# Kernel tuning notes

Hardware: AMD Instinct MI355X
Metric: run time of the kernel (lower is better)

The kernel has to match this reference:

```python
import jax, jax.numpy as jnp
import numpy as np

B, S, E, H = 4, 2048, 2048, 16
D = E // H  # 128


def _rope(x, sin, cos):
    # x: (B, S, H, D); sin/cos: (S, D//2)
    x1, x2 = jnp.split(x, 2, axis=-1)
    c = cos[None, :, None, :]
    s = sin[None, :, None, :]
    return jnp.concatenate([x1 * c - x2 * s, x1 * s + x2 * c], axis=-1)


def setup_inputs() -> dict:
    key = jax.random.key(0)
    ks = jax.random.split(key, 12)
    inp = {
        "x_q": jax.random.normal(ks[0], (B, S, E), jnp.float32),
        "x_kv": jax.random.normal(ks[1], (B, S, E), jnp.float32),
        "Wq": jax.random.normal(ks[2], (E, E), jnp.float32) / np.sqrt(E),
        "bq": jnp.zeros((E,), jnp.float32),
        "Wk": jax.random.normal(ks[3], (E, E), jnp.float32) / np.sqrt(E),
        "bk": jnp.zeros((E,), jnp.float32),
        "Wv": jax.random.normal(ks[4], (E, E), jnp.float32) / np.sqrt(E),
        "bv": jnp.zeros((E,), jnp.float32),
        "Wo": jax.random.normal(ks[5], (E, E), jnp.float32) / np.sqrt(E),
        "bo": jnp.zeros((E,), jnp.float32),
        "angles": jax.random.uniform(ks[6], (2, S, D // 2), jnp.float32),
        "attn_mask": jnp.ones((B, S), jnp.int32),
        "causal": 0,
        "k_rope": 1,
    }
    return inp


def reference(x_q, x_kv, Wq, bq, Wk, bk, Wv, bv, Wo, bo, angles, attn_mask, causal, k_rope):
    sin, cos = angles[0], angles[1]
    q = (x_q @ Wq.T + bq).reshape(B, S, H, D)
    k = (x_kv @ Wk.T + bk).reshape(B, S, H, D)
    v = (x_kv @ Wv.T + bv).reshape(B, S, H, D)
    q = _rope(q, sin, cos)
    if k_rope:
        k = _rope(k, sin, cos)
    # scaled dot-product attention, heads leading: (B, H, S, S)
    scores = jnp.einsum("bqhd,bkhd->bhqk", q, k) / np.sqrt(D).astype(np.float32)
    mask = attn_mask.astype(bool)[:, None, None, :]  # (B,1,1,S_kv)
    if causal:
        cm = jnp.tril(jnp.ones((S, S), bool))[None, None]
        mask = mask & cm
    scores = jnp.where(mask, scores, jnp.finfo(scores.dtype).min)
    probs = jax.nn.softmax(scores, axis=-1)
    attn = jnp.einsum("bhqk,bkhd->bqhd", probs, v).reshape(B, S, E)
    return attn @ Wo.T + bo
```

## Files before the change

### kernel.cpp

```cpp
#include <hip/hip_runtime.h>
#include <hip/hip_bf16.h>


typedef __bf16 bf16;
typedef __bf16 bf16x8 __attribute__((ext_vector_type(8)));
typedef __bf16 bf16x4 __attribute__((ext_vector_type(4)));
typedef __bf16 bf16x2 __attribute__((ext_vector_type(2)));
typedef float  f32x4  __attribute__((ext_vector_type(4)));
typedef float  f32x16 __attribute__((ext_vector_type(16)));

constexpr int Bc = 4, Sc = 2048, Ec = 2048, Hc = 16, Dc = 128;
constexpr int Mc = Bc * Sc;

__device__ __forceinline__ void async16(const void* g, void* l) {
  __builtin_amdgcn_global_load_lds(
      (const __attribute__((address_space(1))) void*)g,
      (__attribute__((address_space(3))) void*)l, 16, 0, 0);
}

__device__ __forceinline__ unsigned int pkbf(float a, float b) {
  union { bf16x2 v; unsigned int u; } c;
  c.v[0] = (bf16)a; c.v[1] = (bf16)b;
  return c.u;
}

__device__ __forceinline__ int swzb32(int r, int kb) {
  int b = r * 64 + kb;
  return b ^ (((b >> 9) & 1) << 5);
}

__global__ void cvt_multi(const float* s0, const float* s1, const float* s2, const float* s3,
                          bf16* d0, bf16* d1, bf16* d2, bf16* d3, int n8) {
  const float* src; bf16* dst;
  switch (blockIdx.y) {
    case 0:  src = s0; dst = d0; break;
    case 1:  src = s1; dst = d1; break;
    case 2:  src = s2; dst = d2; break;
    default: src = s3; dst = d3; break;
  }
  int i = blockIdx.x * blockDim.x + threadIdx.x;
  const int stride = gridDim.x * blockDim.x;
  for (; i < n8; i += stride) {
    const float4 a = *((const float4*)src + (size_t)i * 2);
    const float4 b = *((const float4*)src + (size_t)i * 2 + 1);
    bf16x8 o;
    o[0] = (bf16)a.x; o[1] = (bf16)a.y; o[2] = (bf16)a.z; o[3] = (bf16)a.w;
    o[4] = (bf16)b.x; o[5] = (bf16)b.y; o[6] = (bf16)b.z; o[7] = (bf16)b.w;
    *(bf16x8*)(dst + (size_t)i * 8) = o;
  }
}

template <int OUT_BF16>
__global__ __launch_bounds__(512, 2) void gemm8(
    const bf16* __restrict__ A, const bf16* __restrict__ Bm,
    const float* __restrict__ bias, void* __restrict__ Cout, int Mblocks)
{
  __shared__ __align__(16) bf16 lds[3 * 16384];
  const int tid = threadIdx.x;
  const int w = tid >> 6, lane = tid & 63;
  const int l15 = lane & 15, l16 = lane >> 4;
  const int wm = w >> 2, wn = w & 3;
  const int id = blockIdx.x;
  const int nwg = Mblocks * 8, cpx = nwg >> 3;
  const int swz = (id & 7) * cpx + (id >> 3);
  const int by = swz >> 3, bx = swz & 7;
  const long m0 = (long)by * 256, n0 = (long)bx * 256;
  constexpr int NT = 64;

  auto stA = [&](int buf, long kt, int j) {
    int c = w * 128 + j * 64 + lane;
    int cs = c ^ (((c >> 5) & 1) << 1);
    async16(A + (m0 + (cs >> 2)) * 2048 + kt + (cs & 3) * 8,
            &lds[buf * 16384 + c * 8]);
  };
  auto stB = [&](int buf, long kt, int j) {
    int c = w * 128 + j * 64 + lane;
    int cs = c ^ (((c >> 5) & 1) << 1);
    async16(Bm + (n0 + (cs >> 2)) * 2048 + kt + (cs & 3) * 8,
            &lds[buf * 16384 + 8192 + c * 8]);
  };

  f32x4 acc[8][4];
#pragma unroll
  for (int a = 0; a < 8; ++a)
#pragma unroll
    for (int b = 0; b < 4; ++b) acc[a][b] = f32x4{0.f, 0.f, 0.f, 0.f};

  stA(0, 0, 0); stA(0, 0, 1); stB(0, 0, 0); stB(0, 0, 1);
  stA(1, 32, 0); stA(1, 32, 1); stB(1, 32, 0); stB(1, 32, 1);
  asm volatile("s_waitcnt vmcnt(4)" ::: "memory");
  __builtin_amdgcn_s_barrier();

  int cur = 0, nx = 2;
  for (int t = 0; t < NT; ++t) {
    const char* Ab = (const char*)&lds[cur * 16384];
    const char* Bb = Ab + 16384;
    const long ktn = (long)(t + 2) * 32;
    const bool pf = (t < NT - 2);

    bf16x8 af[8], bf0[2];
#pragma unroll
    for (int mf = 0; mf < 8; ++mf)
      af[mf] = *(const bf16x8*)(Ab + swzb32(wm * 128 + mf * 16 + l15, l16 * 16));
#pragma unroll
    for (int nf = 0; nf < 2; ++nf)
      bf0[nf] = *(const bf16x8*)(Bb + swzb32(wn * 64 + nf * 16 + l15, l16 * 16));
    if (pf) { stA(nx, ktn, 0); stA(nx, ktn, 1); }
    asm volatile("" ::: "memory");
    __builtin_amdgcn_s_barrier();
    __builtin_amdgcn_s_setprio(1);
#pragma unroll
    for (int mf = 0; mf < 8; ++mf)
#pragma unroll
      for (int nf = 0; nf < 2; ++nf)
        acc[mf][nf] = __builtin_amdgcn_mfma_f32_16x16x32_bf16(af[mf], bf0[nf], acc[mf][nf], 0, 0, 0);
    __builtin_amdgcn_s_setprio(0);
    __builtin_amdgcn_s_barrier();

    bf16x8 bf1[2];
#pragma unroll
    for (int nf = 0; nf < 2; ++nf)
      bf1[nf] = *(const bf16x8*)(Bb + swzb32(wn * 64 + (2 + nf) * 16 + l15, l16 * 16));
    if (pf) { stB(nx, ktn, 0); stB(nx, ktn, 1); }
    asm volatile("" ::: "memory");
    __builtin_amdgcn_s_barrier();
    __builtin_amdgcn_s_setprio(1);
#pragma unroll
    for (int mf = 0; mf < 8; ++mf)
#pragma unroll
      for (int nf = 0; nf < 2; ++nf)
        acc[mf][2 + nf] = __builtin_amdgcn_mfma_f32_16x16x32_bf16(af[mf], bf1[nf], acc[mf][2 + nf], 0, 0, 0);
    __builtin_amdgcn_s_setprio(0);
    if (t < NT - 2)       { asm volatile("s_waitcnt vmcnt(4)" ::: "memory"); }
    else if (t == NT - 2) { asm volatile("s_waitcnt vmcnt(0)" ::: "memory"); }
    __builtin_amdgcn_s_barrier();
    cur = (cur == 2) ? 0 : cur + 1;
    nx  = (nx  == 2) ? 0 : nx  + 1;
  }

#pragma unroll
  for (int mf = 0; mf < 8; ++mf)
#pragma unroll
    for (int nf = 0; nf < 4; ++nf) {
      const long m = m0 + wm * 128 + mf * 16 + l16 * 4;
      const long n = n0 + wn * 64 + nf * 16 + l15;
      const float bv = bias[n];
#pragma unroll
      for (int i = 0; i < 4; ++i) {
        float v = acc[mf][nf][i] + bv;
        if (OUT_BF16) ((bf16*)Cout)[(m + i) * 2048 + n] = (bf16)v;
        else          ((float*)Cout)[(m + i) * 2048 + n] = v;
      }
    }
}

__global__ void rope_kernel(bf16* __restrict__ x, const float* __restrict__ angles,
                            const int* __restrict__ flag, int force)
{
  if (!force && flag[0] == 0) return;
  const int t = threadIdx.x;
  const long R = (long)blockIdx.x * 64 + (t >> 2);
  const int d0 = (t & 3) * 16;
  const long s = (R / Hc) % Sc;
  bf16* rowp = x + R * Dc;
  bf16x8 lo0 = *(bf16x8*)(rowp + d0);
  bf16x8 lo1 = *(bf16x8*)(rowp + d0 + 8);
  bf16x8 hi0 = *(bf16x8*)(rowp + d0 + 64);
  bf16x8 hi1 = *(bf16x8*)(rowp + d0 + 72);
  const float* sp = angles + s * 64 + d0;
  const float* cp = angles + 131072 + s * 64 + d0;
  bf16x8 a0, a1, b0, b1;
#pragma unroll
  for (int j = 0; j < 8; ++j) {
    float c = cp[j], sn = sp[j];
    float x1 = (float)lo0[j], x2 = (float)hi0[j];
    a0[j] = (bf16)(x1 * c - x2 * sn);
    b0[j] = (bf16)(x1 * sn + x2 * c);
    float c1 = cp[j + 8], sn1 = sp[j + 8];
    float y1 = (float)lo1[j], y2 = (float)hi1[j];
    a1[j] = (bf16)(y1 * c1 - y2 * sn1);
    b1[j] = (bf16)(y1 * sn1 + y2 * c1);
  }
  *(bf16x8*)(rowp + d0)      = a0;
  *(bf16x8*)(rowp + d0 + 8)  = a1;
  *(bf16x8*)(rowp + d0 + 64) = b0;
  *(bf16x8*)(rowp + d0 + 72) = b1;
}

__global__ void transpose_v(const bf16* __restrict__ v0, bf16* __restrict__ Vt)
{
  __shared__ __align__(16) bf16 T[64 * 128];
  const int t = threadIdx.x;
  const int bh = blockIdx.y, b = bh >> 4, h = bh & 15;
  const int s0 = blockIdx.x * 64;
#pragma unroll
  for (int it = 0; it < 4; ++it) {
    int slot = it * 256 + t;
    int r = slot >> 4, g = slot & 15;
    async16(v0 + ((size_t)(b * Sc + s0 + r) * Hc + h) * Dc + ((g ^ (r & 15)) << 3),
            &T[slot * 8]);
  }
  __syncthreads();
  const int d = t >> 1, half = t & 1;
  bf16x8 pk[4];
#pragma unroll
  for (int j = 0; j < 32; ++j) {
    int sl = half * 32 + j;
    pk[j >> 3][j & 7] = T[sl * 128 + (((d >> 3) ^ (sl & 15)) << 3) + (d & 7)];
  }
  bf16* op = Vt + ((size_t)bh * Dc + d) * Sc + s0 + half * 32;
#pragma unroll
  for (int v = 0; v < 4; ++v) *(bf16x8*)(op + v * 8) = pk[v];
}

__global__ __launch_bounds__(256, 2) void attn_kernel(
    const bf16* __restrict__ q0, const bf16* __restrict__ k0,
    const bf16* __restrict__ vt, const int* __restrict__ mask,
    const int* __restrict__ causal_p, const float* __restrict__ angles,
    bf16* __restrict__ attn_out)
{
  __shared__ __align__(16) bf16 Ks[2][64 * 128];
  __shared__ __align__(16) bf16 Vs[2][128 * 64];

  const int tid = threadIdx.x, wid = tid >> 6, lane = tid & 63;
  const int l31 = lane & 31, h = lane >> 5;
  const int id = blockIdx.x;
  const int swz = (id & 7) * 128 + (id >> 3);
  const int bh = swz >> 4, qb = swz & 15;
  const int b = bh >> 4, hh = bh & 15;
  const int q_glob = qb * 128 + wid * 32 + l31;
  const int causal_f = causal_p[0];
  const float SC = 0.08838834764831845f * 1.4426950408889634f;
  const float NEG = -3.0e38f;

  auto stageKV = [&](int kv0s, int bufs) {
#pragma unroll
    for (int it = 0; it < 4; ++it) {
      int g = it * 256 + tid;
      int r = g >> 4, gp = g & 15;
      async16(k0 + ((size_t)(b * Sc + kv0s + r) * Hc + hh) * Dc + ((gp ^ (r & 15)) << 3),
              &Ks[bufs][g * 8]);
    }
#pragma unroll
    for (int it = 0; it < 4; ++it) {
      int g = it * 256 + tid;
      int r = g >> 3, gp = g & 7;
      async16(vt + ((size_t)bh * Dc + r) * Sc + kv0s + ((gp ^ (r & 7)) << 3),
              &Vs[bufs][g * 8]);
    }
  };

  bf16x8 qf[8];
  {
    const bf16* qrow = q0 + ((size_t)(b * Sc + q_glob) * Hc + hh) * Dc;
#pragma unroll
    for (int dc = 0; dc < 4; ++dc) {
      bf16x8 lo = *(const bf16x8*)(qrow + dc * 16 + h * 8);
      bf16x8 hi = *(const bf16x8*)(qrow + (dc + 4) * 16 + h * 8);
      const float* sp = angles + (size_t)q_glob * 64 + dc * 16 + h * 8;
      union { float4 v[2]; float f[8]; } sn, cs;
      sn.v[0] = ((const float4*)sp)[0];
      sn.v[1] = ((const float4*)sp)[1];
      cs.v[0] = ((const float4*)(sp + 131072))[0];
      cs.v[1] = ((const float4*)(sp + 131072))[1];
#pragma unroll
      for (int j = 0; j < 8; ++j) {
        float x1 = (float)lo[j], x2 = (float)hi[j];
        qf[dc][j]     = (bf16)(SC * (x1 * cs.f[j] - x2 * sn.f[j]));
        qf[dc + 4][j] = (bf16)(SC * (x1 * sn.f[j] + x2 * cs.f[j]));
      }
    }
  }

  f32x16 o[4];
#pragma unroll
  for (int db = 0; db < 4; ++db)
#pragma unroll
    for (int r = 0; r < 16; ++r) o[db][r] = 0.f;
  float mrun = NEG, lrun = 0.f;

  stageKV(0, 0);
  const int mv0 = mask[b * Sc + lane];
  asm volatile("s_waitcnt vmcnt(0)" ::: "memory");
  __builtin_amdgcn_s_barrier();
  unsigned long long mbits = __ballot(mv0 != 0);
  int cur = 0;

  for (int kv0 = 0; kv0 < Sc; kv0 += 64) {
    const int kvn = kv0 + 64;
    unsigned long long mbits_next = ~0ull;
    if (kvn < Sc) {
      const int mvn = mask[b * Sc + kvn + lane];
      mbits_next = __ballot(mvn != 0);
      stageKV(kvn, cur ^ 1);
    }

#pragma unroll
    for (int kvb = 0; kvb < 2; ++kvb) {
      f32x16 s;
#pragma unroll
      for (int r = 0; r < 16; ++r) s[r] = 0.f;
      __builtin_amdgcn_s_setprio(1);
#pragma unroll
      for (int dc = 0; dc < 8; ++dc) {
        bf16x8 kf = *(const bf16x8*)&Ks[cur][(kvb * 32 + l31) * 128 +
                                           (((dc * 2 + h) ^ (l31 & 15)) << 3)];
        s = __builtin_amdgcn_mfma_f32_32x32x16_bf16(kf, qf[dc], s, 0, 0, 0);
      }
      __builtin_amdgcn_s_setprio(0);
      if (mbits != ~0ull) {
#pragma unroll
        for (int r = 0; r < 16; ++r) {
          int off = kvb * 32 + (r & 3) + 8 * (r >> 2) + 4 * h;
          if (!((mbits >> off) & 1)) s[r] = NEG;
        }
      }
      if (causal_f) {
#pragma unroll
        for (int r = 0; r < 16; ++r) {
          int kvg = kv0 + kvb * 32 + (r & 3) + 8 * (r >> 2) + 4 * h;
          if (kvg > q_glob) s[r] = NEG;
        }
      }
      float tmax = s[0];
#pragma unroll
      for (int r = 1; r < 16; ++r) tmax = fmaxf(tmax, s[r]);
      tmax = fmaxf(tmax, __shfl_xor(tmax, 32));
      if (!__all(tmax <= mrun + 8.0f)) {
        const float mnew = fmaxf(mrun, tmax);
        const float alpha = __builtin_amdgcn_exp2f(mrun - mnew);
#pragma unroll
        for (int db = 0; db < 4; ++db)
#pragma unroll
          for (int r = 0; r < 16; ++r) o[db][r] *= alpha;
        lrun *= alpha;
        mrun = mnew;
      }
      float rs = 0.f;
#pragma unroll
      for (int r = 0; r < 16; ++r) {
        s[r] = __builtin_amdgcn_exp2f(s[r] - mrun);
        rs += s[r];
      }
      rs += __shfl_xor(rs, 32);
      lrun += rs;
      unsigned int dw0 = pkbf(s[0], s[1]),   dw1 = pkbf(s[2], s[3]);
      unsigned int dw2 = pkbf(s[4], s[5]),   dw3 = pkbf(s[6], s[7]);
      unsigned int dw4 = pkbf(s[8], s[9]),   dw5 = pkbf(s[10], s[11]);
      unsigned int dw6 = pkbf(s[12], s[13]), dw7 = pkbf(s[14], s[15]);
      asm volatile("v_permlane32_swap_b32 %0, %1" : "+v"(dw0), "+v"(dw2));
      asm volatile("v_permlane32_swap_b32 %0, %1" : "+v"(dw1), "+v"(dw3));
      asm volatile("v_permlane32_swap_b32 %0, %1" : "+v"(dw4), "+v"(dw6));
      asm volatile("v_permlane32_swap_b32 %0, %1" : "+v"(dw5), "+v"(dw7));
      union { unsigned int u[4]; bf16x8 v; } pf0, pf1;
      pf0.u[0] = dw0; pf0.u[1] = dw1; pf0.u[2] = dw2; pf0.u[3] = dw3;
      pf1.u[0] = dw4; pf1.u[1] = dw5; pf1.u[2] = dw6; pf1.u[3] = dw7;
      __builtin_amdgcn_s_setprio(1);
#pragma unroll
      for (int ksb = 0; ksb < 2; ++ksb) {
        const bf16x8 pfv = ksb ? pf1.v : pf0.v;
#pragma unroll
        for (int db = 0; db < 4; ++db) {
          const int dr = db * 32 + l31;
          bf16x8 vb = *(const bf16x8*)&Vs[cur][dr * 64 +
                          ((((kvb * 2 + ksb) * 2 + h) ^ (dr & 7)) << 3)];
          o[db] = __builtin_amdgcn_mfma_f32_32x32x16_bf16(vb, pfv, o[db], 0, 0, 0);
        }
      }
      __builtin_amdgcn_s_setprio(0);
    }

    asm volatile("s_waitcnt vmcnt(0)" ::: "memory");
    __builtin_amdgcn_s_barrier();
    cur ^= 1;
    mbits = mbits_next;
  }

  const float inv = 1.0f / lrun;
  bf16* orow = attn_out + ((size_t)(b * Sc + q_glob) * Hc + hh) * Dc;
#pragma unroll
  for (int db = 0; db < 4; ++db)
#pragma unroll
    for (int rq = 0; rq < 4; ++rq) {
      bf16x4 st;
#pragma unroll
      for (int i = 0; i < 4; ++i) st[i] = (bf16)(o[db][rq * 4 + i] * inv);
      *(bf16x4*)(orow + db * 32 + rq * 8 + 4 * h) = st;
    }
}

extern "C" void kernel_launch(void* const* d_in, const int* in_sizes, int n_in,
                              void* d_out, int out_size, void* d_ws, size_t ws_size,
                              hipStream_t stream)
{
  const float* x_q    = (const float*)d_in[0];
  const float* x_kv   = (const float*)d_in[1];
  const float* Wq     = (const float*)d_in[2];
  const float* bq     = (const float*)d_in[3];
  const float* Wk     = (const float*)d_in[4];
  const float* bk     = (const float*)d_in[5];
  const float* Wv     = (const float*)d_in[6];
  const float* bv     = (const float*)d_in[7];
  const float* Wo     = (const float*)d_in[8];
  const float* bo     = (const float*)d_in[9];
  const float* angles = (const float*)d_in[10];
  const int*   amask  = (const int*)d_in[11];
  const int*   causal = (const int*)d_in[12];
  const int*   k_rope = (const int*)d_in[13];
  float* out = (float*)d_out;

  char* ws = (char*)d_ws;
  const size_t MB32 = (size_t)33554432;
  bf16* xq16  = (bf16*)(ws);
  bf16* xkv16 = (bf16*)(ws + MB32);
  bf16* wq16  = (bf16*)(ws + 2 * MB32);
  bf16* wk16  = wq16 + 4194304;
  bf16* wv16  = wk16 + 4194304;
  bf16* wo16  = wv16 + 4194304;
  bf16* q0    = (bf16*)(ws + 3 * MB32);
  bf16* k0    = (bf16*)(ws + 4 * MB32);
  bf16* v0    = (bf16*)(ws + 5 * MB32);
  bf16* Vt     = xq16;
  bf16* attn16 = xkv16;

  cvt_multi<<<dim3(1024, 2), 256, 0, stream>>>(x_q, x_kv, x_q, x_kv,
                                               xq16, xkv16, xq16, xkv16, Mc * Ec / 8);
  cvt_multi<<<dim3(256, 4), 256, 0, stream>>>(Wq, Wk, Wv, Wo,
                                              wq16, wk16, wv16, wo16, Ec * Ec / 8);

  const int gemmBlocks = (Mc / 256) * (Ec / 256);
  gemm8<1><<<gemmBlocks, 512, 0, stream>>>(xq16,  wq16, bq, q0, Mc / 256);
  gemm8<1><<<gemmBlocks, 512, 0, stream>>>(xkv16, wk16, bk, k0, Mc / 256);
  gemm8<1><<<gemmBlocks, 512, 0, stream>>>(xkv16, wv16, bv, v0, Mc / 256);

  rope_kernel<<<2048, 256, 0, stream>>>(k0, angles, k_rope, 0);
  transpose_v<<<dim3(Sc / 64, Bc * Hc), 256, 0, stream>>>(v0, Vt);

  attn_kernel<<<1024, 256, 0, stream>>>(q0, k0, Vt, amask, causal, angles, attn16);

  gemm8<0><<<gemmBlocks, 512, 0, stream>>>(attn16, wo16, bo, out, Mc / 256);
}
```

Measured before the change: 531.9 us.

## Fuse V transpose into GEMM epilogue, deepen GEMM pipeline, restage attention V

The V projection GEMM now writes its output directly in head-major transposed layout, which removes the separate transpose kernel and the intermediate V buffer round trip. The GEMM prefetch ring grows from three to four LDS stages to hide more load latency. The attention kernel now single-buffers V, staging it per tile and waiting on it only after the first QK/softmax chunk, which cuts LDS use so the kernel can target three blocks per CU. In exchange, the transposed epilogue issues strided 8-byte stores, and the 128KB GEMM LDS footprint may no longer allow two blocks per CU.

Measured after the change: 864.7 us. +62.6%, slower.

```diff
diff --git a/kernel.cpp b/kernel.cpp
--- a/kernel.cpp
+++ b/kernel.cpp
@@ -50,12 +50,12 @@
   }
 }
 
-template <int OUT_BF16>
+template <int OUT>
 __global__ __launch_bounds__(512, 2) void gemm8(
     const bf16* __restrict__ A, const bf16* __restrict__ Bm,
     const float* __restrict__ bias, void* __restrict__ Cout, int Mblocks)
 {
-  __shared__ __align__(16) bf16 lds[3 * 16384];
+  __shared__ __align__(16) bf16 lds[4 * 16384];
   const int tid = threadIdx.x;
   const int w = tid >> 6, lane = tid & 63;
   const int l15 = lane & 15, l16 = lane >> 4;
@@ -86,17 +86,18 @@
 #pragma unroll
     for (int b = 0; b < 4; ++b) acc[a][b] = f32x4{0.f, 0.f, 0.f, 0.f};
 
-  stA(0, 0, 0); stA(0, 0, 1); stB(0, 0, 0); stB(0, 0, 1);
+  stA(0, 0, 0);  stA(0, 0, 1);  stB(0, 0, 0);  stB(0, 0, 1);
   stA(1, 32, 0); stA(1, 32, 1); stB(1, 32, 0); stB(1, 32, 1);
-  asm volatile("s_waitcnt vmcnt(4)" ::: "memory");
+  stA(2, 64, 0); stA(2, 64, 1); stB(2, 64, 0); stB(2, 64, 1);
+  asm volatile("s_waitcnt vmcnt(8)" ::: "memory");
   __builtin_amdgcn_s_barrier();
 
-  int cur = 0, nx = 2;
+  int cur = 0, nx = 3;
   for (int t = 0; t < NT; ++t) {
     const char* Ab = (const char*)&lds[cur * 16384];
     const char* Bb = Ab + 16384;
-    const long ktn = (long)(t + 2) * 32;
-    const bool pf = (t < NT - 2);
+    const long ktn = (long)(t + 3) * 32;
+    const bool pf = (t < NT - 3);
 
     bf16x8 af[8], bf0[2];
 #pragma unroll
@@ -131,11 +132,12 @@
       for (int nf = 0; nf < 2; ++nf)
         acc[mf][2 + nf] = __builtin_amdgcn_mfma_f32_16x16x32_bf16(af[mf], bf1[nf], acc[mf][2 + nf], 0, 0, 0);
     __builtin_amdgcn_s_setprio(0);
-    if (t < NT - 2)       { asm volatile("s_waitcnt vmcnt(4)" ::: "memory"); }
+    if (t < NT - 3)       { asm volatile("s_waitcnt vmcnt(8)" ::: "memory"); }
+    else if (t == NT - 3) { asm volatile("s_waitcnt vmcnt(4)" ::: "memory"); }
     else if (t == NT - 2) { asm volatile("s_waitcnt vmcnt(0)" ::: "memory"); }
     __builtin_amdgcn_s_barrier();
-    cur = (cur == 2) ? 0 : cur + 1;
-    nx  = (nx  == 2) ? 0 : nx  + 1;
+    cur = (cur + 1) & 3;
+    nx  = (nx + 1) & 3;
   }
 
 #pragma unroll
@@ -145,11 +147,20 @@
       const long m = m0 + wm * 128 + mf * 16 + l16 * 4;
       const long n = n0 + wn * 64 + nf * 16 + l15;
       const float bv = bias[n];
-#pragma unroll
-      for (int i = 0; i < 4; ++i) {
-        float v = acc[mf][nf][i] + bv;
-        if (OUT_BF16) ((bf16*)Cout)[(m + i) * 2048 + n] = (bf16)v;
-        else          ((float*)Cout)[(m + i) * 2048 + n] = v;
+      if (OUT == 2) {
+        const long bb = m >> 11, ss = m & 2047;
+        const long head = n >> 7, d = n & 127;
+        bf16x4 st;
+#pragma unroll
+        for (int i = 0; i < 4; ++i) st[i] = (bf16)(acc[mf][nf][i] + bv);
+        *(bf16x4*)((bf16*)Cout + ((((bb << 4) + head) << 7) + d) * 2048 + ss) = st;
+      } else {
+#pragma unroll
+        for (int i = 0; i < 4; ++i) {
+          float v = acc[mf][nf][i] + bv;
+          if (OUT == 1) ((bf16*)Cout)[(m + i) * 2048 + n] = (bf16)v;
+          else          ((float*)Cout)[(m + i) * 2048 + n] = v;
+        }
       }
     }
 }
@@ -187,40 +198,14 @@
   *(bf16x8*)(rowp + d0 + 72) = b1;
 }
 
-__global__ void transpose_v(const bf16* __restrict__ v0, bf16* __restrict__ Vt)
-{
-  __shared__ __align__(16) bf16 T[64 * 128];
-  const int t = threadIdx.x;
-  const int bh = blockIdx.y, b = bh >> 4, h = bh & 15;
-  const int s0 = blockIdx.x * 64;
-#pragma unroll
-  for (int it = 0; it < 4; ++it) {
-    int slot = it * 256 + t;
-    int r = slot >> 4, g = slot & 15;
-    async16(v0 + ((size_t)(b * Sc + s0 + r) * Hc + h) * Dc + ((g ^ (r & 15)) << 3),
-            &T[slot * 8]);
-  }
-  __syncthreads();
-  const int d = t >> 1, half = t & 1;
-  bf16x8 pk[4];
-#pragma unroll
-  for (int j = 0; j < 32; ++j) {
-    int sl = half * 32 + j;
-    pk[j >> 3][j & 7] = T[sl * 128 + (((d >> 3) ^ (sl & 15)) << 3) + (d & 7)];
-  }
-  bf16* op = Vt + ((size_t)bh * Dc + d) * Sc + s0 + half * 32;
-#pragma unroll
-  for (int v = 0; v < 4; ++v) *(bf16x8*)(op + v * 8) = pk[v];
-}
-
-__global__ __launch_bounds__(256, 2) void attn_kernel(
+__global__ __launch_bounds__(256, 3) void attn_kernel(
     const bf16* __restrict__ q0, const bf16* __restrict__ k0,
     const bf16* __restrict__ vt, const int* __restrict__ mask,
     const int* __restrict__ causal_p, const float* __restrict__ angles,
     bf16* __restrict__ attn_out)
 {
   __shared__ __align__(16) bf16 Ks[2][64 * 128];
-  __shared__ __align__(16) bf16 Vs[2][128 * 64];
+  __shared__ __align__(16) bf16 Vs[128 * 64];
 
   const int tid = threadIdx.x, wid = tid >> 6, lane = tid & 63;
   const int l31 = lane & 31, h = lane >> 5;
@@ -233,7 +218,7 @@
   const float SC = 0.08838834764831845f * 1.4426950408889634f;
   const float NEG = -3.0e38f;
 
-  auto stageKV = [&](int kv0s, int bufs) {
+  auto stageK = [&](int kv0s, int bufs) {
 #pragma unroll
     for (int it = 0; it < 4; ++it) {
       int g = it * 256 + tid;
@@ -241,12 +226,14 @@
       async16(k0 + ((size_t)(b * Sc + kv0s + r) * Hc + hh) * Dc + ((gp ^ (r & 15)) << 3),
               &Ks[bufs][g * 8]);
     }
+  };
+  auto stageV = [&](int kv0s) {
 #pragma unroll
     for (int it = 0; it < 4; ++it) {
       int g = it * 256 + tid;
       int r = g >> 3, gp = g & 7;
       async16(vt + ((size_t)bh * Dc + r) * Sc + kv0s + ((gp ^ (r & 7)) << 3),
-              &Vs[bufs][g * 8]);
+              &Vs[g * 8]);
     }
   };
 
@@ -279,96 +266,108 @@
     for (int r = 0; r < 16; ++r) o[db][r] = 0.f;
   float mrun = NEG, lrun = 0.f;
 
-  stageKV(0, 0);
+  stageK(0, 0);
   const int mv0 = mask[b * Sc + lane];
   asm volatile("s_waitcnt vmcnt(0)" ::: "memory");
   __builtin_amdgcn_s_barrier();
   unsigned long long mbits = __ballot(mv0 != 0);
   int cur = 0;
 
+  union pfu { unsigned int u[4]; bf16x8 v; };
+  auto qk_sm_pack = [&](int kv0_, int kvb, unsigned long long mb, pfu& pf0, pfu& pf1) {
+    f32x16 s;
+#pragma unroll
+    for (int r = 0; r < 16; ++r) s[r] = 0.f;
+    __builtin_amdgcn_s_setprio(1);
+#pragma unroll
+    for (int dc = 0; dc < 8; ++dc) {
+      bf16x8 kf = *(const bf16x8*)&Ks[cur][(kvb * 32 + l31) * 128 +
+                                         (((dc * 2 + h) ^ (l31 & 15)) << 3)];
+      s = __builtin_amdgcn_mfma_f32_32x32x16_bf16(kf, qf[dc], s, 0, 0, 0);
+    }
+    __builtin_amdgcn_s_setprio(0);
+    if (mb != ~0ull) {
+#pragma unroll
+      for (int r = 0; r < 16; ++r) {
+        int off = kvb * 32 + (r & 3) + 8 * (r >> 2) + 4 * h;
+        if (!((mb >> off) & 1)) s[r] = NEG;
+      }
+    }
+    if (causal_f) {
+#pragma unroll
+      for (int r = 0; r < 16; ++r) {
+        int kvg = kv0_ + kvb * 32 + (r & 3) + 8 * (r >> 2) + 4 * h;
+        if (kvg > q_glob) s[r] = NEG;
+      }
+    }
+    float tmax = s[0];
+#pragma unroll
+    for (int r = 1; r < 16; ++r) tmax = fmaxf(tmax, s[r]);
+    tmax = fmaxf(tmax, __shfl_xor(tmax, 32));
+    if (!__all(tmax <= mrun + 8.0f)) {
+      const float mnew = fmaxf(mrun, tmax);
+      const float alpha = __builtin_amdgcn_exp2f(mrun - mnew);
+#pragma unroll
+      for (int db = 0; db < 4; ++db)
+#pragma unroll
+        for (int r = 0; r < 16; ++r) o[db][r] *= alpha;
+      lrun *= alpha;
+      mrun = mnew;
+    }
+    float rs = 0.f;
+#pragma unroll
+    for (int r = 0; r < 16; ++r) {
+      s[r] = __builtin_amdgcn_exp2f(s[r] - mrun);
+      rs += s[r];
+    }
+    rs += __shfl_xor(rs, 32);
+    lrun += rs;
+    unsigned int dw0 = pkbf(s[0], s[1]),   dw1 = pkbf(s[2], s[3]);
+    unsigned int dw2 = pkbf(s[4], s[5]),   dw3 = pkbf(s[6], s[7]);
+    unsigned int dw4 = pkbf(s[8], s[9]),   dw5 = pkbf(s[10], s[11]);
+    unsigned int dw6 = pkbf(s[12], s[13]), dw7 = pkbf(s[14], s[15]);
+    asm volatile("v_permlane32_swap_b32 %0, %1" : "+v"(dw0), "+v"(dw2));
+    asm volatile("v_permlane32_swap_b32 %0, %1" : "+v"(dw1), "+v"(dw3));
+    asm volatile("v_permlane32_swap_b32 %0, %1" : "+v"(dw4), "+v"(dw6));
+    asm volatile("v_permlane32_swap_b32 %0, %1" : "+v"(dw5), "+v"(dw7));
+    pf0.u[0] = dw0; pf0.u[1] = dw1; pf0.u[2] = dw2; pf0.u[3] = dw3;
+    pf1.u[0] = dw4; pf1.u[1] = dw5; pf1.u[2] = dw6; pf1.u[3] = dw7;
+  };
+  auto pv = [&](int kvb, const pfu& pf0, const pfu& pf1) {
+    __builtin_amdgcn_s_setprio(1);
+#pragma unroll
+    for (int ksb = 0; ksb < 2; ++ksb) {
+      const bf16x8 pfv = ksb ? pf1.v : pf0.v;
+#pragma unroll
+      for (int db = 0; db < 4; ++db) {
+        const int dr = db * 32 + l31;
+        bf16x8 vb = *(const bf16x8*)&Vs[dr * 64 +
+                        ((((kvb * 2 + ksb) * 2 + h) ^ (dr & 7)) << 3)];
+        o[db] = __builtin_amdgcn_mfma_f32_32x32x16_bf16(vb, pfv, o[db], 0, 0, 0);
+      }
+    }
+    __builtin_amdgcn_s_setprio(0);
+  };
+
   for (int kv0 = 0; kv0 < Sc; kv0 += 64) {
     const int kvn = kv0 + 64;
+    const bool has_next = (kvn < Sc);
     unsigned long long mbits_next = ~0ull;
-    if (kvn < Sc) {
+    if (has_next) {
       const int mvn = mask[b * Sc + kvn + lane];
       mbits_next = __ballot(mvn != 0);
-      stageKV(kvn, cur ^ 1);
-    }
-
-#pragma unroll
-    for (int kvb = 0; kvb < 2; ++kvb) {
-      f32x16 s;
-#pragma unroll
-      for (int r = 0; r < 16; ++r) s[r] = 0.f;
-      __builtin_amdgcn_s_setprio(1);
-#pragma unroll
-      for (int dc = 0; dc < 8; ++dc) {
-        bf16x8 kf = *(const bf16x8*)&Ks[cur][(kvb * 32 + l31) * 128 +
-                                           (((dc * 2 + h) ^ (l31 & 15)) << 3)];
-        s = __builtin_amdgcn_mfma_f32_32x32x16_bf16(kf, qf[dc], s, 0, 0, 0);
-      }
-      __builtin_amdgcn_s_setprio(0);
-      if (mbits != ~0ull) {
-#pragma unroll
-        for (int r = 0; r < 16; ++r) {
-          int off = kvb * 32 + (r & 3) + 8 * (r >> 2) + 4 * h;
-          if (!((mbits >> off) & 1)) s[r] = NEG;
-        }
-      }
-      if (causal_f) {
-#pragma unroll
-        for (int r = 0; r < 16; ++r) {
-          int kvg = kv0 + kvb * 32 + (r & 3) + 8 * (r >> 2) + 4 * h;
-          if (kvg > q_glob) s[r] = NEG;
-        }
-      }
-      float tmax = s[0];
-#pragma unroll
-      for (int r = 1; r < 16; ++r) tmax = fmaxf(tmax, s[r]);
-      tmax = fmaxf(tmax, __shfl_xor(tmax, 32));
-      if (!__all(tmax <= mrun + 8.0f)) {
-        const float mnew = fmaxf(mrun, tmax);
-        const float alpha = __builtin_amdgcn_exp2f(mrun - mnew);
-#pragma unroll
-        for (int db = 0; db < 4; ++db)
-#pragma unroll
-          for (int r = 0; r < 16; ++r) o[db][r] *= alpha;
-        lrun *= alpha;
-        mrun = mnew;
-      }
-      float rs = 0.f;
-#pragma unroll
-      for (int r = 0; r < 16; ++r) {
-        s[r] = __builtin_amdgcn_exp2f(s[r] - mrun);
-        rs += s[r];
-      }
-      rs += __shfl_xor(rs, 32);
-      lrun += rs;
-      unsigned int dw0 = pkbf(s[0], s[1]),   dw1 = pkbf(s[2], s[3]);
-      unsigned int dw2 = pkbf(s[4], s[5]),   dw3 = pkbf(s[6], s[7]);
-      unsigned int dw4 = pkbf(s[8], s[9]),   dw5 = pkbf(s[10], s[11]);
-      unsigned int dw6 = pkbf(s[12], s[13]), dw7 = pkbf(s[14], s[15]);
-      asm volatile("v_permlane32_swap_b32 %0, %1" : "+v"(dw0), "+v"(dw2));
-      asm volatile("v_permlane32_swap_b32 %0, %1" : "+v"(dw1), "+v"(dw3));
-      asm volatile("v_permlane32_swap_b32 %0, %1" : "+v"(dw4), "+v"(dw6));
-      asm volatile("v_permlane32_swap_b32 %0, %1" : "+v"(dw5), "+v"(dw7));
-      union { unsigned int u[4]; bf16x8 v; } pf0, pf1;
-      pf0.u[0] = dw0; pf0.u[1] = dw1; pf0.u[2] = dw2; pf0.u[3] = dw3;
-      pf1.u[0] = dw4; pf1.u[1] = dw5; pf1.u[2] = dw6; pf1.u[3] = dw7;
-      __builtin_amdgcn_s_setprio(1);
-#pragma unroll
-      for (int ksb = 0; ksb < 2; ++ksb) {
-        const bf16x8 pfv = ksb ? pf1.v : pf0.v;
-#pragma unroll
-        for (int db = 0; db < 4; ++db) {
-          const int dr = db * 32 + l31;
-          bf16x8 vb = *(const bf16x8*)&Vs[cur][dr * 64 +
-                          ((((kvb * 2 + ksb) * 2 + h) ^ (dr & 7)) << 3)];
-          o[db] = __builtin_amdgcn_mfma_f32_32x32x16_bf16(vb, pfv, o[db], 0, 0, 0);
-        }
-      }
-      __builtin_amdgcn_s_setprio(0);
-    }
+    }
+    stageV(kv0);
+    if (has_next) stageK(kvn, cur ^ 1);
+
+    pfu a0, a1, b0, b1;
+    qk_sm_pack(kv0, 0, mbits, a0, a1);
+    if (has_next) { asm volatile("s_waitcnt vmcnt(4)" ::: "memory"); }
+    else          { asm volatile("s_waitcnt vmcnt(0)" ::: "memory"); }
+    __builtin_amdgcn_s_barrier();
+    pv(0, a0, a1);
+    qk_sm_pack(kv0, 1, mbits, b0, b1);
+    pv(1, b0, b1);
 
     asm volatile("s_waitcnt vmcnt(0)" ::: "memory");
     __builtin_amdgcn_s_barrier();
@@ -419,7 +418,6 @@
   bf16* wo16  = wv16 + 4194304;
   bf16* q0    = (bf16*)(ws + 3 * MB32);
   bf16* k0    = (bf16*)(ws + 4 * MB32);
-  bf16* v0    = (bf16*)(ws + 5 * MB32);
   bf16* Vt     = xq16;
   bf16* attn16 = xkv16;
 
@@ -431,10 +429,9 @@
   const int gemmBlocks = (Mc / 256) * (Ec / 256);
   gemm8<1><<<gemmBlocks, 512, 0, stream>>>(xq16,  wq16, bq, q0, Mc / 256);
   gemm8<1><<<gemmBlocks, 512, 0, stream>>>(xkv16, wk16, bk, k0, Mc / 256);
-  gemm8<1><<<gemmBlocks, 512, 0, stream>>>(xkv16, wv16, bv, v0, Mc / 256);
+  gemm8<2><<<gemmBlocks, 512, 0, stream>>>(xkv16, wv16, bv, Vt, Mc / 256);
 
   rope_kernel<<<2048, 256, 0, stream>>>(k0, angles, k_rope, 0);
-  transpose_v<<<dim3(Sc / 64, Bc * Hc), 256, 0, stream>>>(v0, Vt);
 
   attn_kernel<<<1024, 256, 0, stream>>>(q0, k0, Vt, amask, causal, angles, attn16);
 
```
